# Kernel optimization log

Measured on AMD Instinct MI355X. Metric: run time of the kernel, lower is better.

The kernel has to match this reference:

```python
import jax, jax.numpy as jnp
import numpy as np

ATTEN = 2  # window half-size -> 2*ATTEN+1 = 5 neighbors
B, S, IN, H, MID, OUT = 1024, 100, 100, 128, 32, 2
MAX_LEN = 100
SQRT_H = float(np.sqrt(float(H)))


def _xavier(k, i, o):
    return jax.random.normal(k, (i, o), jnp.float32) * np.sqrt(2.0 / (i + o))


def _positional_encoding():
    pos = np.arange(MAX_LEN, dtype=np.float32)[:, None]
    div = np.exp(np.arange(0, H, 2, dtype=np.float32) * (-np.log(10000.0) / H))
    pe = np.zeros((MAX_LEN, H), np.float32)
    pe[:, 0::2] = np.sin(pos * div)
    pe[:, 1::2] = np.cos(pos * div)
    return jnp.asarray(pe[None])  # (1, MAX_LEN, H)


def setup_inputs() -> dict:
    key = jax.random.key(0)
    ks = jax.random.split(key, 7)
    return {
        "x": jax.random.normal(ks[0], (B, S, IN), jnp.float32),
        "W1": _xavier(ks[1], IN, H),
        "b1": jnp.zeros((1, 1, H), jnp.float32),
        "Wq": _xavier(ks[2], H, H),
        "Wk": _xavier(ks[3], H, H),
        "Wv": _xavier(ks[4], H, H),
        "bv": jnp.zeros((1, 1, H), jnp.float32),
        "W2": _xavier(ks[5], H, MID),
        "b2": jnp.zeros((1, 1, MID), jnp.float32),
        "W3": _xavier(ks[6], MID, OUT),
        "b3": jnp.zeros((1, 1, OUT), jnp.float32),
        "pe": _positional_encoding(),
    }


def reference(x, W1, b1, Wq, Wk, Wv, bv, W2, b2, W3, b3, pe):
    seq_len = x.shape[1]
    h = jax.nn.relu(x @ W1 + b1) + pe[:, :seq_len, :]  # (B,S,H)
    # zero-pad seq dim by ATTEN on each side; torch pad+roll+stack+slice is
    # equivalent to gathering window offsets +2,+1,0,-1,-2 (in that order)
    padded = jnp.pad(h, ((0, 0), (ATTEN, ATTEN), (0, 0)))
    x_nei = jnp.stack(
        [padded[:, ATTEN - k: ATTEN - k + seq_len, :] for k in range(-ATTEN, ATTEN + 1)],
        axis=2,
    )  # (B,S,5,H); index m corresponds to neighbor x[i + ATTEN - m]
    q = h @ Wq                      # (B,S,H)
    keys = x_nei @ Wk               # (B,S,5,H)
    vals = x_nei @ Wv + bv          # (B,S,5,H)
    scores = jnp.einsum("bsh,bswh->bsw", q, keys) / SQRT_H
    w = jax.nn.softmax(scores, axis=-1)  # (B,S,5)
    context = jnp.einsum("bsw,bswh->bsh", w, vals)
    output = jax.nn.relu(context @ W2 + b2) @ W3 + b3  # (B,S,OUT)
    return output, w[:, :, None, :]  # weights shaped (B,S,1,5) like torch
```

## Files before the change

kernel.cpp:

```cpp
#include <hip/hip_runtime.h>
#include <hip/hip_bf16.h>

#define B_ 1024
#define S_ 100
#define IN_ 100
#define H_ 128
#define MID_ 32
#define OUT_ 2
#define P_ (B_ * S_)
#define RSQRT_H 0.08838834764831845f
#define LSTR 136
#define MROWS 112

typedef __attribute__((ext_vector_type(8))) short short8;
typedef __attribute__((ext_vector_type(4))) float float4v;

__device__ __forceinline__ float bf2f(ushort u) {
    union { unsigned u; float f; } c; c.u = ((unsigned)u) << 16; return c.f;
}
__device__ __forceinline__ ushort f2bf(float x) {
    union { float f; unsigned u; } c; c.f = x;
    unsigned r = c.u + 0x7FFFu + ((c.u >> 16) & 1u);
    return (ushort)(r >> 16);
}

__global__ __launch_bounds__(256) void prep_transpose(const float* __restrict__ W1,
                                                      const float* __restrict__ Wv,
                                                      const float* __restrict__ W2,
                                                      ushort* __restrict__ W1T,
                                                      ushort* __restrict__ WvT,
                                                      ushort* __restrict__ W2T) {
    int g = blockIdx.x * 256 + threadIdx.x;
    if (g < 16384) {
        int n = g >> 7, k = g & 127;
        W1T[g] = (k < IN_) ? f2bf(W1[k * H_ + n]) : (ushort)0;
    } else if (g < 32768) {
        int e = g - 16384; int n = e >> 7, k = e & 127;
        WvT[e] = f2bf(Wv[k * H_ + n]);
    } else {
        int e = g - 32768; int n = e >> 7, k = e & 127;
        W2T[e] = f2bf(W2[k * MID_ + n]);
    }
}

__global__ __launch_bounds__(256) void prep_wqk(const float* __restrict__ Wq,
                                                const float* __restrict__ Wk,
                                                ushort* __restrict__ WqkT) {
    __shared__ float sq[32][132];
    __shared__ float sk[32][132];
    int n0 = (blockIdx.x >> 2) * 32, k0 = (blockIdx.x & 3) * 32;
    int tid = threadIdx.x;
    for (int i = tid; i < 32 * 128; i += 256) {
        int r = i >> 7, c = i & 127;
        sq[r][c] = Wq[(k0 + r) * H_ + c];
        sk[r][c] = Wk[(n0 + r) * H_ + c];
    }
    __syncthreads();
    for (int i = tid; i < 1024; i += 256) {
        int kk = i & 31, nn = i >> 5;
        float a = 0.f;
        for (int j = 0; j < 128; ++j) a += sq[kk][j] * sk[nn][j];
        WqkT[(n0 + nn) * 128 + (k0 + kk)] = f2bf(a);
    }
}

template <int EPI>
__device__ __forceinline__ void mm_stage(const ushort* __restrict__ A_lds,
                                         const ushort* __restrict__ WT,
                                         ushort* __restrict__ C_lds,
                                         int wave, int lane,
                                         const float* __restrict__ bias,
                                         const float* __restrict__ pe) {
    int l15 = lane & 15, quad = lane >> 4;
    short8 bfrag[2][4];
#pragma unroll
    for (int nt = 0; nt < 2; ++nt) {
        int n = (wave * 2 + nt) * 16 + l15;
#pragma unroll
        for (int ks = 0; ks < 4; ++ks)
            bfrag[nt][ks] = *(const short8*)(WT + n * 128 + ks * 32 + quad * 8);
    }
    float biasv[2] = {0.f, 0.f};
    if (EPI != 0) {
#pragma unroll
        for (int nt = 0; nt < 2; ++nt) biasv[nt] = bias[(wave * 2 + nt) * 16 + l15];
    }
#pragma unroll
    for (int mt = 0; mt < 7; ++mt) {
        short8 afrag[4];
#pragma unroll
        for (int ks = 0; ks < 4; ++ks)
            afrag[ks] = *(const short8*)(A_lds + (mt * 16 + l15) * LSTR + ks * 32 + quad * 8);
#pragma unroll
        for (int nt = 0; nt < 2; ++nt) {
            float4v acc = {0.f, 0.f, 0.f, 0.f};
#pragma unroll
            for (int ks = 0; ks < 4; ++ks)
                acc = __builtin_amdgcn_mfma_f32_16x16x32_bf16(afrag[ks], bfrag[nt][ks], acc, 0, 0, 0);
            int n = (wave * 2 + nt) * 16 + l15;
#pragma unroll
            for (int i = 0; i < 4; ++i) {
                int row = mt * 16 + quad * 4 + i;
                float v = acc[i];
                if (EPI == 1) v = (row < S_) ? (fmaxf(v + biasv[nt], 0.f) + pe[row * H_ + n]) : 0.f;
                else if (EPI == 2) v = v + biasv[nt];
                C_lds[row * LSTR + n] = f2bf(v);
            }
        }
    }
}

__global__ __launch_bounds__(256) void fused_kernel(
    const float* __restrict__ x, const ushort* __restrict__ W1T,
    const ushort* __restrict__ WqkT, const ushort* __restrict__ WvT,
    const ushort* __restrict__ W2T,
    const float* __restrict__ b1, const float* __restrict__ bv,
    const float* __restrict__ b2, const float* __restrict__ W3,
    const float* __restrict__ b3, const float* __restrict__ pe,
    float* __restrict__ out, float* __restrict__ wout) {
    __shared__ ushort klds[MROWS * LSTR];
    __shared__ ushort xh[MROWS * LSTR];
    int tid = threadIdx.x, wave = tid >> 6, lane = tid & 63;
    int b = blockIdx.x;
    const float* xb = x + (size_t)b * (S_ * IN_);

    for (int i = tid; i < MROWS * LSTR; i += 256) klds[i] = 0;
    __syncthreads();
    for (int i = tid; i < S_ * IN_; i += 256) {
        int m = i / IN_, k = i - m * IN_;
        klds[m * LSTR + k] = f2bf(xb[i]);
    }
    __syncthreads();
    mm_stage<1>(klds, W1T, xh, wave, lane, b1, pe);
    __syncthreads();
    mm_stage<0>(xh, WqkT, klds, wave, lane, nullptr, nullptr);
    __syncthreads();
    if (tid < 2 * S_) {
        int r = tid >> 1, half = tid & 1;
        const ushort* kqr = klds + r * LSTR + half * 64;
        float kqf[64];
#pragma unroll
        for (int c = 0; c < 8; ++c) {
            short8 v = *(const short8*)(kqr + c * 8);
#pragma unroll
            for (int j = 0; j < 8; ++j) kqf[c * 8 + j] = bf2f((ushort)v[j]);
        }
        float sc[5];
#pragma unroll
        for (int m = 0; m < 5; ++m) {
            int nr = r + 2 - m;
            float p = 0.f;
            if (nr >= 0 && nr < S_) {
                const ushort* hr = xh + nr * LSTR + half * 64;
#pragma unroll
                for (int c = 0; c < 8; ++c) {
                    short8 v = *(const short8*)(hr + c * 8);
#pragma unroll
                    for (int j = 0; j < 8; ++j) p += bf2f((ushort)v[j]) * kqf[c * 8 + j];
                }
            }
            sc[m] = p;
        }
#pragma unroll
        for (int m = 0; m < 5; ++m)
            sc[m] = (sc[m] + __shfl_xor(sc[m], 1)) * RSQRT_H;
        float mx = sc[0];
#pragma unroll
        for (int m = 1; m < 5; ++m) mx = fmaxf(mx, sc[m]);
        float e[5], ss = 0.f;
#pragma unroll
        for (int m = 0; m < 5; ++m) { e[m] = expf(sc[m] - mx); ss += e[m]; }
        float inv = 1.f / ss;
        float w5[5];
#pragma unroll
        for (int m = 0; m < 5; ++m) w5[m] = e[m] * inv;
        if (half == 0) {
            float* wp = wout + (size_t)b * (S_ * 5) + r * 5;
#pragma unroll
            for (int m = 0; m < 5; ++m) wp[m] = w5[m];
        }
        float acc[64];
#pragma unroll
        for (int c = 0; c < 64; ++c) acc[c] = 0.f;
#pragma unroll
        for (int m = 0; m < 5; ++m) {
            int nr = r + 2 - m;
            if (nr < 0 || nr >= S_) continue;
            float wm = w5[m];
            const ushort* hr = xh + nr * LSTR + half * 64;
#pragma unroll
            for (int c = 0; c < 8; ++c) {
                short8 v = *(const short8*)(hr + c * 8);
#pragma unroll
                for (int j = 0; j < 8; ++j) acc[c * 8 + j] += wm * bf2f((ushort)v[j]);
            }
        }
        ushort* op = klds + r * LSTR + half * 64;
#pragma unroll
        for (int c = 0; c < 8; ++c) {
            short8 v;
#pragma unroll
            for (int j = 0; j < 8; ++j) v[j] = (short)f2bf(acc[c * 8 + j]);
            *(short8*)(op + c * 8) = v;
        }
    }
    __syncthreads();
    mm_stage<2>(klds, WvT, xh, wave, lane, bv, nullptr);
    __syncthreads();
    {
        int l15 = lane & 15, quad = lane >> 4;
        short8 bfrag[2][4];
#pragma unroll
        for (int nt = 0; nt < 2; ++nt)
#pragma unroll
            for (int ks = 0; ks < 4; ++ks)
                bfrag[nt][ks] = *(const short8*)(W2T + (nt * 16 + l15) * 128 + ks * 32 + quad * 8);
        float biasv[2] = {b2[l15], b2[16 + l15]};
        for (int mt = wave; mt < 7; mt += 4) {
            short8 afrag[4];
#pragma unroll
            for (int ks = 0; ks < 4; ++ks)
                afrag[ks] = *(const short8*)(xh + (mt * 16 + l15) * LSTR + ks * 32 + quad * 8);
#pragma unroll
            for (int nt = 0; nt < 2; ++nt) {
                float4v acc = {0.f, 0.f, 0.f, 0.f};
#pragma unroll
                for (int ks = 0; ks < 4; ++ks)
                    acc = __builtin_amdgcn_mfma_f32_16x16x32_bf16(afrag[ks], bfrag[nt][ks], acc, 0, 0, 0);
#pragma unroll
                for (int i = 0; i < 4; ++i) {
                    int row = mt * 16 + quad * 4 + i;
                    klds[row * LSTR + nt * 16 + l15] = f2bf(fmaxf(acc[i] + biasv[nt], 0.f));
                }
            }
        }
    }
    __syncthreads();
    if (tid < S_) {
        int r = tid;
        float o0 = b3[0], o1 = b3[1];
#pragma unroll
        for (int k = 0; k < MID_; ++k) {
            float mv = bf2f(klds[r * LSTR + k]);
            o0 += mv * W3[k * 2];
            o1 += mv * W3[k * 2 + 1];
        }
        float* op = out + (size_t)b * (S_ * OUT_) + r * OUT_;
        op[0] = o0; op[1] = o1;
    }
}

extern "C" void kernel_launch(void* const* d_in, const int* in_sizes, int n_in,
                              void* d_out, int out_size, void* d_ws, size_t ws_size,
                              hipStream_t stream) {
    const float* x  = (const float*)d_in[0];
    const float* W1 = (const float*)d_in[1];
    const float* b1 = (const float*)d_in[2];
    const float* Wq = (const float*)d_in[3];
    const float* Wk = (const float*)d_in[4];
    const float* Wv = (const float*)d_in[5];
    const float* bv = (const float*)d_in[6];
    const float* W2 = (const float*)d_in[7];
    const float* b2 = (const float*)d_in[8];
    const float* W3 = (const float*)d_in[9];
    const float* b3 = (const float*)d_in[10];
    const float* pe = (const float*)d_in[11];

    float* out  = (float*)d_out;
    float* wout = out + (size_t)P_ * OUT_;

    ushort* W1T  = (ushort*)d_ws;
    ushort* WqkT = W1T + 16384;
    ushort* WvT  = WqkT + 16384;
    ushort* W2T  = WvT + 16384;

    prep_transpose<<<144, 256, 0, stream>>>(W1, Wv, W2, W1T, WvT, W2T);
    prep_wqk<<<16, 256, 0, stream>>>(Wq, Wk, WqkT);
    fused_kernel<<<B_, 256, 0, stream>>>(x, W1T, WqkT, WvT, W2T,
                                         b1, bv, b2, W3, b3, pe, out, wout);
}
```

Baseline: 150.6 us.

## Split each batch sequence into four row tiles with halo recompute

The fused kernel now launches four blocks per batch element, each handling 25 sequence rows plus a 2-row halo on each side. This shrinks LDS use and raises occupancy through launch bounds. The attention stage is spread across 8 threads per row instead of 2, and the two prep kernels are merged into one launch. The cost is that the first matmul is recomputed on the halo rows, and each block pads to 32 MFMA rows for only 25 useful ones.

```diff
diff --git a/kernel.cpp b/kernel.cpp
--- a/kernel.cpp
+++ b/kernel.cpp
@@ -10,7 +10,9 @@
 #define P_ (B_ * S_)
 #define RSQRT_H 0.08838834764831845f
 #define LSTR 136
-#define MROWS 112
+#define TILE 25
+#define KR 32
+#define HR 34
 
 typedef __attribute__((ext_vector_type(8))) short short8;
 typedef __attribute__((ext_vector_type(4))) float float4v;
@@ -24,53 +26,55 @@
     return (ushort)(r >> 16);
 }
 
-__global__ __launch_bounds__(256) void prep_transpose(const float* __restrict__ W1,
-                                                      const float* __restrict__ Wv,
-                                                      const float* __restrict__ W2,
-                                                      ushort* __restrict__ W1T,
-                                                      ushort* __restrict__ WvT,
-                                                      ushort* __restrict__ W2T) {
-    int g = blockIdx.x * 256 + threadIdx.x;
-    if (g < 16384) {
-        int n = g >> 7, k = g & 127;
-        W1T[g] = (k < IN_) ? f2bf(W1[k * H_ + n]) : (ushort)0;
-    } else if (g < 32768) {
-        int e = g - 16384; int n = e >> 7, k = e & 127;
-        WvT[e] = f2bf(Wv[k * H_ + n]);
+__global__ __launch_bounds__(256) void prep_kernel(const float* __restrict__ W1,
+                                                   const float* __restrict__ Wv,
+                                                   const float* __restrict__ W2,
+                                                   const float* __restrict__ Wq,
+                                                   const float* __restrict__ Wk,
+                                                   ushort* __restrict__ W1T,
+                                                   ushort* __restrict__ WvT,
+                                                   ushort* __restrict__ W2T,
+                                                   ushort* __restrict__ WqkT) {
+    int tid = threadIdx.x;
+    if (blockIdx.x < 144) {
+        int g = blockIdx.x * 256 + tid;
+        if (g < 16384) {
+            int n = g >> 7, k = g & 127;
+            W1T[g] = (k < IN_) ? f2bf(W1[k * H_ + n]) : (ushort)0;
+        } else if (g < 32768) {
+            int e = g - 16384; int n = e >> 7, k = e & 127;
+            WvT[e] = f2bf(Wv[k * H_ + n]);
+        } else {
+            int e = g - 32768; int n = e >> 7, k = e & 127;
+            W2T[e] = f2bf(W2[k * MID_ + n]);
+        }
     } else {
-        int e = g - 32768; int n = e >> 7, k = e & 127;
-        W2T[e] = f2bf(W2[k * MID_ + n]);
-    }
-}
-
-__global__ __launch_bounds__(256) void prep_wqk(const float* __restrict__ Wq,
-                                                const float* __restrict__ Wk,
-                                                ushort* __restrict__ WqkT) {
-    __shared__ float sq[32][132];
-    __shared__ float sk[32][132];
-    int n0 = (blockIdx.x >> 2) * 32, k0 = (blockIdx.x & 3) * 32;
-    int tid = threadIdx.x;
-    for (int i = tid; i < 32 * 128; i += 256) {
-        int r = i >> 7, c = i & 127;
-        sq[r][c] = Wq[(k0 + r) * H_ + c];
-        sk[r][c] = Wk[(n0 + r) * H_ + c];
-    }
-    __syncthreads();
-    for (int i = tid; i < 1024; i += 256) {
-        int kk = i & 31, nn = i >> 5;
-        float a = 0.f;
-        for (int j = 0; j < 128; ++j) a += sq[kk][j] * sk[nn][j];
-        WqkT[(n0 + nn) * 128 + (k0 + kk)] = f2bf(a);
+        __shared__ float sq[32][132];
+        __shared__ float sk[32][132];
+        int bb = blockIdx.x - 144;
+        int n0 = (bb >> 2) * 32, k0 = (bb & 3) * 32;
+        for (int i = tid; i < 32 * 128; i += 256) {
+            int r = i >> 7, c = i & 127;
+            sq[r][c] = Wq[(k0 + r) * H_ + c];
+            sk[r][c] = Wk[(n0 + r) * H_ + c];
+        }
+        __syncthreads();
+        for (int i = tid; i < 1024; i += 256) {
+            int kk = i & 31, nn = i >> 5;
+            float a = 0.f;
+            for (int j = 0; j < 128; ++j) a += sq[kk][j] * sk[nn][j];
+            WqkT[(n0 + nn) * 128 + (k0 + kk)] = f2bf(a);
+        }
     }
 }
 
 template <int EPI>
-__device__ __forceinline__ void mm_stage(const ushort* __restrict__ A_lds,
-                                         const ushort* __restrict__ WT,
-                                         ushort* __restrict__ C_lds,
-                                         int wave, int lane,
-                                         const float* __restrict__ bias,
-                                         const float* __restrict__ pe) {
+__device__ __forceinline__ void mm2(const ushort* __restrict__ A, int abase,
+                                    const ushort* __restrict__ WT,
+                                    ushort* __restrict__ C,
+                                    int wave, int lane,
+                                    const float* __restrict__ bias,
+                                    const float* __restrict__ pe, int srow0) {
     int l15 = lane & 15, quad = lane >> 4;
     short8 bfrag[2][4];
 #pragma unroll
@@ -86,11 +90,11 @@
         for (int nt = 0; nt < 2; ++nt) biasv[nt] = bias[(wave * 2 + nt) * 16 + l15];
     }
 #pragma unroll
-    for (int mt = 0; mt < 7; ++mt) {
+    for (int mt = 0; mt < 2; ++mt) {
         short8 afrag[4];
 #pragma unroll
         for (int ks = 0; ks < 4; ++ks)
-            afrag[ks] = *(const short8*)(A_lds + (mt * 16 + l15) * LSTR + ks * 32 + quad * 8);
+            afrag[ks] = *(const short8*)(A + (abase + mt * 16 + l15) * LSTR + ks * 32 + quad * 8);
 #pragma unroll
         for (int nt = 0; nt < 2; ++nt) {
             float4v acc = {0.f, 0.f, 0.f, 0.f};
@@ -102,15 +106,18 @@
             for (int i = 0; i < 4; ++i) {
                 int row = mt * 16 + quad * 4 + i;
                 float v = acc[i];
-                if (EPI == 1) v = (row < S_) ? (fmaxf(v + biasv[nt], 0.f) + pe[row * H_ + n]) : 0.f;
-                else if (EPI == 2) v = v + biasv[nt];
-                C_lds[row * LSTR + n] = f2bf(v);
+                if (EPI == 1) {
+                    int srow = srow0 + row;
+                    v = (srow >= 0 && srow < S_)
+                            ? (fmaxf(v + biasv[nt], 0.f) + pe[srow * H_ + n]) : 0.f;
+                } else if (EPI == 2) v = v + biasv[nt];
+                C[row * LSTR + n] = f2bf(v);
             }
         }
     }
 }
 
-__global__ __launch_bounds__(256) void fused_kernel(
+__global__ __launch_bounds__(256, 5) void fused_kernel(
     const float* __restrict__ x, const ushort* __restrict__ W1T,
     const ushort* __restrict__ WqkT, const ushort* __restrict__ WvT,
     const ushort* __restrict__ W2T,
@@ -118,29 +125,52 @@
     const float* __restrict__ b2, const float* __restrict__ W3,
     const float* __restrict__ b3, const float* __restrict__ pe,
     float* __restrict__ out, float* __restrict__ wout) {
-    __shared__ ushort klds[MROWS * LSTR];
-    __shared__ ushort xh[MROWS * LSTR];
+    __shared__ ushort klds[KR * LSTR];
+    __shared__ ushort hlds[HR * LSTR];
+    __shared__ float warr[TILE * 5];
+
     int tid = threadIdx.x, wave = tid >> 6, lane = tid & 63;
-    int b = blockIdx.x;
-    const float* xb = x + (size_t)b * (S_ * IN_);
-
-    for (int i = tid; i < MROWS * LSTR; i += 256) klds[i] = 0;
-    __syncthreads();
-    for (int i = tid; i < S_ * IN_; i += 256) {
-        int m = i / IN_, k = i - m * IN_;
-        klds[m * LSTR + k] = f2bf(xb[i]);
-    }
-    __syncthreads();
-    mm_stage<1>(klds, W1T, xh, wave, lane, b1, pe);
-    __syncthreads();
-    mm_stage<0>(xh, WqkT, klds, wave, lane, nullptr, nullptr);
-    __syncthreads();
-    if (tid < 2 * S_) {
-        int r = tid >> 1, half = tid & 1;
-        const ushort* kqr = klds + r * LSTR + half * 64;
-        float kqf[64];
-#pragma unroll
-        for (int c = 0; c < 8; ++c) {
+    int b = blockIdx.x >> 2, t = blockIdx.x & 3;
+    int r0 = t * TILE;
+    int srow0 = r0 - 2;
+
+    for (int i = tid; i < 29 * 18; i += 256) {
+        int r = i / 18, c = 100 + 2 * (i - r * 18);
+        *(uint*)(klds + r * LSTR + c) = 0u;
+    }
+    for (int i = tid; i < 3 * 68; i += 256) {
+        int r = 29 + i / 68, c = 2 * (i % 68);
+        *(uint*)(klds + r * LSTR + c) = 0u;
+    }
+    for (int i = tid; i < 2 * 68; i += 256) {
+        int r = 32 + i / 68, c = 2 * (i % 68);
+        *(uint*)(hlds + r * LSTR + c) = 0u;
+    }
+    {
+        int g0 = srow0 < 0 ? 0 : srow0;
+        int g1 = (r0 + 27 < S_) ? (r0 + 27) : S_;
+        int lr0 = g0 - srow0;
+        const float* xb = x + ((size_t)b * S_ + g0) * IN_;
+        int pairs = (g1 - g0) * 50;
+        for (int p = tid; p < pairs; p += 256) {
+            int row = p / 50;
+            int c2 = (p - row * 50) * 2;
+            const float* src = xb + row * IN_ + c2;
+            uint pk = ((uint)f2bf(src[1]) << 16) | (uint)f2bf(src[0]);
+            *(uint*)(klds + (lr0 + row) * LSTR + c2) = pk;
+        }
+    }
+    __syncthreads();
+    mm2<1>(klds, 0, W1T, hlds, wave, lane, b1, pe, srow0);
+    __syncthreads();
+    mm2<0>(hlds, 2, WqkT, klds, wave, lane, nullptr, nullptr, 0);
+    __syncthreads();
+    if (tid < TILE * 8) {
+        int r = tid >> 3, sub = tid & 7;
+        const ushort* kqr = klds + r * LSTR + sub * 16;
+        float kqf[16];
+#pragma unroll
+        for (int c = 0; c < 2; ++c) {
             short8 v = *(const short8*)(kqr + c * 8);
 #pragma unroll
             for (int j = 0; j < 8; ++j) kqf[c * 8 + j] = bf2f((ushort)v[j]);
@@ -148,12 +178,12 @@
         float sc[5];
 #pragma unroll
         for (int m = 0; m < 5; ++m) {
-            int nr = r + 2 - m;
+            int gs = r0 + r + 2 - m;
             float p = 0.f;
-            if (nr >= 0 && nr < S_) {
-                const ushort* hr = xh + nr * LSTR + half * 64;
-#pragma unroll
-                for (int c = 0; c < 8; ++c) {
+            if (gs >= 0 && gs < S_) {
+                const ushort* hr = hlds + (r + 4 - m) * LSTR + sub * 16;
+#pragma unroll
+                for (int c = 0; c < 2; ++c) {
                     short8 v = *(const short8*)(hr + c * 8);
 #pragma unroll
                     for (int j = 0; j < 8; ++j) p += bf2f((ushort)v[j]) * kqf[c * 8 + j];
@@ -162,42 +192,45 @@
             sc[m] = p;
         }
 #pragma unroll
-        for (int m = 0; m < 5; ++m)
-            sc[m] = (sc[m] + __shfl_xor(sc[m], 1)) * RSQRT_H;
+        for (int m = 0; m < 5; ++m) {
+            sc[m] += __shfl_xor(sc[m], 1);
+            sc[m] += __shfl_xor(sc[m], 2);
+            sc[m] += __shfl_xor(sc[m], 4);
+            sc[m] *= RSQRT_H;
+        }
         float mx = sc[0];
 #pragma unroll
         for (int m = 1; m < 5; ++m) mx = fmaxf(mx, sc[m]);
         float e[5], ss = 0.f;
 #pragma unroll
-        for (int m = 0; m < 5; ++m) { e[m] = expf(sc[m] - mx); ss += e[m]; }
+        for (int m = 0; m < 5; ++m) { e[m] = __expf(sc[m] - mx); ss += e[m]; }
         float inv = 1.f / ss;
         float w5[5];
 #pragma unroll
         for (int m = 0; m < 5; ++m) w5[m] = e[m] * inv;
-        if (half == 0) {
-            float* wp = wout + (size_t)b * (S_ * 5) + r * 5;
-#pragma unroll
-            for (int m = 0; m < 5; ++m) wp[m] = w5[m];
-        }
-        float acc[64];
-#pragma unroll
-        for (int c = 0; c < 64; ++c) acc[c] = 0.f;
+        if (sub == 0) {
+#pragma unroll
+            for (int m = 0; m < 5; ++m) warr[r * 5 + m] = w5[m];
+        }
+        float acc[16];
+#pragma unroll
+        for (int c = 0; c < 16; ++c) acc[c] = 0.f;
 #pragma unroll
         for (int m = 0; m < 5; ++m) {
-            int nr = r + 2 - m;
-            if (nr < 0 || nr >= S_) continue;
+            int gs = r0 + r + 2 - m;
+            if (gs < 0 || gs >= S_) continue;
             float wm = w5[m];
-            const ushort* hr = xh + nr * LSTR + half * 64;
-#pragma unroll
-            for (int c = 0; c < 8; ++c) {
+            const ushort* hr = hlds + (r + 4 - m) * LSTR + sub * 16;
+#pragma unroll
+            for (int c = 0; c < 2; ++c) {
                 short8 v = *(const short8*)(hr + c * 8);
 #pragma unroll
                 for (int j = 0; j < 8; ++j) acc[c * 8 + j] += wm * bf2f((ushort)v[j]);
             }
         }
-        ushort* op = klds + r * LSTR + half * 64;
-#pragma unroll
-        for (int c = 0; c < 8; ++c) {
+        ushort* op = klds + r * LSTR + sub * 16;
+#pragma unroll
+        for (int c = 0; c < 2; ++c) {
             short8 v;
 #pragma unroll
             for (int j = 0; j < 8; ++j) v[j] = (short)f2bf(acc[c * 8 + j]);
@@ -205,38 +238,34 @@
         }
     }
     __syncthreads();
-    mm_stage<2>(klds, WvT, xh, wave, lane, bv, nullptr);
+    if (tid < TILE * 5)
+        wout[(size_t)b * (S_ * 5) + r0 * 5 + tid] = warr[tid];
+    mm2<2>(klds, 0, WvT, hlds, wave, lane, bv, nullptr, 0);
     __syncthreads();
     {
         int l15 = lane & 15, quad = lane >> 4;
-        short8 bfrag[2][4];
-#pragma unroll
-        for (int nt = 0; nt < 2; ++nt)
-#pragma unroll
-            for (int ks = 0; ks < 4; ++ks)
-                bfrag[nt][ks] = *(const short8*)(W2T + (nt * 16 + l15) * 128 + ks * 32 + quad * 8);
-        float biasv[2] = {b2[l15], b2[16 + l15]};
-        for (int mt = wave; mt < 7; mt += 4) {
-            short8 afrag[4];
-#pragma unroll
-            for (int ks = 0; ks < 4; ++ks)
-                afrag[ks] = *(const short8*)(xh + (mt * 16 + l15) * LSTR + ks * 32 + quad * 8);
-#pragma unroll
-            for (int nt = 0; nt < 2; ++nt) {
-                float4v acc = {0.f, 0.f, 0.f, 0.f};
-#pragma unroll
-                for (int ks = 0; ks < 4; ++ks)
-                    acc = __builtin_amdgcn_mfma_f32_16x16x32_bf16(afrag[ks], bfrag[nt][ks], acc, 0, 0, 0);
-#pragma unroll
-                for (int i = 0; i < 4; ++i) {
-                    int row = mt * 16 + quad * 4 + i;
-                    klds[row * LSTR + nt * 16 + l15] = f2bf(fmaxf(acc[i] + biasv[nt], 0.f));
-                }
-            }
-        }
-    }
-    __syncthreads();
-    if (tid < S_) {
+        int mt = wave & 1, nt = wave >> 1;
+        short8 bfrag[4];
+#pragma unroll
+        for (int ks = 0; ks < 4; ++ks)
+            bfrag[ks] = *(const short8*)(W2T + (nt * 16 + l15) * 128 + ks * 32 + quad * 8);
+        float bias2 = b2[nt * 16 + l15];
+        short8 afrag[4];
+#pragma unroll
+        for (int ks = 0; ks < 4; ++ks)
+            afrag[ks] = *(const short8*)(hlds + (mt * 16 + l15) * LSTR + ks * 32 + quad * 8);
+        float4v acc = {0.f, 0.f, 0.f, 0.f};
+#pragma unroll
+        for (int ks = 0; ks < 4; ++ks)
+            acc = __builtin_amdgcn_mfma_f32_16x16x32_bf16(afrag[ks], bfrag[ks], acc, 0, 0, 0);
+#pragma unroll
+        for (int i = 0; i < 4; ++i) {
+            int row = mt * 16 + quad * 4 + i;
+            klds[row * LSTR + nt * 16 + l15] = f2bf(fmaxf(acc[i] + bias2, 0.f));
+        }
+    }
+    __syncthreads();
+    if (tid < TILE) {
         int r = tid;
         float o0 = b3[0], o1 = b3[1];
 #pragma unroll
@@ -245,8 +274,8 @@
             o0 += mv * W3[k * 2];
             o1 += mv * W3[k * 2 + 1];
         }
-        float* op = out + (size_t)b * (S_ * OUT_) + r * OUT_;
-        op[0] = o0; op[1] = o1;
+        float2* op = (float2*)(out + ((size_t)b * S_ + r0 + r) * OUT_);
+        *op = make_float2(o0, o1);
     }
 }
 
@@ -274,8 +303,7 @@
     ushort* WvT  = WqkT + 16384;
     ushort* W2T  = WvT + 16384;
 
-    prep_transpose<<<144, 256, 0, stream>>>(W1, Wv, W2, W1T, WvT, W2T);
-    prep_wqk<<<16, 256, 0, stream>>>(Wq, Wk, WqkT);
-    fused_kernel<<<B_, 256, 0, stream>>>(x, W1T, WqkT, WvT, W2T,
-                                         b1, bv, b2, W3, b3, pe, out, wout);
-}
+    prep_kernel<<<160, 256, 0, stream>>>(W1, Wv, W2, Wq, Wk, W1T, WvT, W2T, WqkT);
+    fused_kernel<<<B_ * 4, 256, 0, stream>>>(x, W1T, WqkT, WvT, W2T,
+                                             b1, bv, b2, W3, b3, pe, out, wout);
+}
```

Result: slower. 163.3 us (+8.4%).
